# Performance work log

Measured on AMD Instinct MI355X. Metric: run time of the kernel, lower is better.

Reference implementation:

```python
import jax, jax.numpy as jnp
import numpy as np

L, B, T, D, V = 4, 32, 512, 512, 1000


def setup_inputs() -> dict:
    key = jax.random.key(0)
    k0, k1, k2, k3, k4 = jax.random.split(key, 5)
    ids = jax.random.randint(k0, (B, T), 0, V)
    mask = jax.random.randint(k1, (B, T), 0, 2).astype(bool)  # True = valid token
    emb = jax.random.normal(k2, (V, D), dtype=jnp.float32) * 0.1
    W = jax.random.normal(k3, (L, D, 3 * D), dtype=jnp.float32) / np.float32(np.sqrt(D))
    v = jax.random.normal(k4, (L, 2, D), dtype=jnp.float32) * 0.1  # (v_f, v_r) per layer
    b = jnp.zeros((L, 2, D), dtype=jnp.float32)                    # (b_f, b_r) per layer
    return {"ids": ids, "mask": mask, "emb": emb, "W": W, "v": v, "b": b}


def _sru_layer(x, pad, Wl, vf, vr, bf, br):
    # x: [T,B,D] layer input; pad: [T,B,1] bool (True = padded step)
    Tn, Bn, Dn = x.shape
    U = jnp.einsum('tbd,de->tbe', x, Wl).reshape(Tn, Bn, 3, Dn)
    xt, fpre, rpre = U[:, :, 0], U[:, :, 1], U[:, :, 2]

    def step(c, inp):
        xt_t, fp_t, rp_t, x_t, pad_t = inp
        f = jax.nn.sigmoid(fp_t + vf * c + bf)
        r = jax.nn.sigmoid(rp_t + vr * c + br)
        c_new = f * c + (1.0 - f) * xt_t
        h = r * jnp.tanh(c_new) + (1.0 - r) * x_t  # highway (input_size==hidden_size)
        c_out = jnp.where(pad_t, c, c_new)          # padded step: keep state
        h = jnp.where(pad_t, 0.0, h)                # padded step: zero output
        return c_out, h

    c0 = jnp.zeros_like(x[0])  # zero initial hidden state, as in the torch code
    _, h = jax.lax.scan(step, c0, (xt, fpre, rpre, x, pad))
    return h  # [T,B,D]


def reference(ids, mask, emb, W, v, b):
    x = emb[ids]                       # CharEmbedder lookup: [B,T,D]
    x = jnp.transpose(x, (1, 0, 2))    # [T,B,D]  (permute(1,0,2))
    pad = (~mask).T[:, :, None]        # inverted_mask.T -> [T,B,1]
    for l in range(L):
        x = _sru_layer(x, pad, W[l], v[l, 0], v[l, 1], b[l, 0], b[l, 1])
    return jnp.transpose(x, (1, 0, 2))  # back to [B,T,D]
```

## Files before the change

### kernel.cpp

```cpp
#include <hip/hip_runtime.h>
#include <hip/hip_bf16.h>


#define LAYERS 4
#define BB 32
#define TT 512
#define DD 512
#define N3 1536
#define MROWS (TT * BB)
#define WPL ((size_t)DD * N3)
#define SB 32
#define LOG2E 1.4426950408889634f
#define TWOLOG2E 2.8853900817779268f

typedef unsigned short u16;
typedef unsigned int u32;
typedef _Float16 half8 __attribute__((ext_vector_type(8)));
typedef float f32x4 __attribute__((ext_vector_type(4)));

#define SBAR() asm volatile("s_barrier" ::: "memory")
#define WAITVM(n) asm volatile("s_waitcnt vmcnt(" n ")" ::: "memory")

__device__ __forceinline__ float b2f(u16 u) {
  union { unsigned int i; float f; } x;
  x.i = ((unsigned int)u) << 16;
  return x.f;
}
__device__ __forceinline__ u16 f2h(float f) {
  _Float16 h = (_Float16)f;
  return *(u16*)&h;
}
__device__ __forceinline__ float h2f(u16 u) {
  _Float16 h;
  *(u16*)&h = u;
  return (float)h;
}
__device__ __forceinline__ float rcpf(float x) { return __builtin_amdgcn_rcpf(x); }
__device__ __forceinline__ float exp2f_(float x) { return __builtin_amdgcn_exp2f(x); }

__device__ __forceinline__ void async_ld16(const void* g, void* l) {
  __builtin_amdgcn_global_load_lds(
      (const __attribute__((address_space(1))) void*)g,
      (__attribute__((address_space(3))) void*)l, 16, 0, 0);
}
__device__ __forceinline__ void async_ld4(const void* g, void* l) {
  __builtin_amdgcn_global_load_lds(
      (const __attribute__((address_space(1))) void*)g,
      (__attribute__((address_space(3))) void*)l, 4, 0, 0);
}

__global__ void detect_kernel(const u16* __restrict__ emb_u,
                              const int* __restrict__ mask_i,
                              const int* __restrict__ ids_i,
                              int* __restrict__ flags) {
  __shared__ int cnt[3];
  __shared__ int zc;
  int tid = threadIdx.x;
  if (tid < 3) cnt[tid] = 0;
  if (tid == 0) zc = 0;
  __syncthreads();
  int bad = 0, zero_even = 0;
  for (int i = tid; i < 8192; i += 256) {
    u16 u = emb_u[i];
    unsigned e = (u >> 7) & 0xFF;
    if (e >= 0x8F) bad++;
    if ((i & 1) == 0 && u == 0) zero_even++;
  }
  if (bad) atomicAdd(&cnt[0], bad);
  if (zero_even) atomicAdd(&zc, zero_even);
  if (tid < 64) {
    unsigned vv = (unsigned)mask_i[tid];
    if (vv > 1u) atomicAdd(&cnt[1], 1);
  }
  if (tid < 256) {
    if (ids_i[2 * tid + 1] == 0) atomicAdd(&cnt[2], 1);
  }
  __syncthreads();
  if (tid == 0) {
    flags[0] = (cnt[0] > 64 || zc > 3000) ? 1 : 0;
    flags[1] = (cnt[1] > 0) ? 1 : 0;
    flags[2] = (cnt[2] >= 192) ? 1 : 0;
  }
}

__global__ __launch_bounds__(256)
void wprep_kernel(const void* __restrict__ W, u16* __restrict__ W16,
                  const int* __restrict__ flags) {
  __shared__ float tileW[32][33];
  int l = blockIdx.z;
  int k0 = blockIdx.x * 32;
  int n0 = blockIdx.y * 32;
  int tx = threadIdx.x & 31;
  int ty = threadIdx.x >> 5;
  int ff = flags[0];
  const float* Wf = (const float*)W + (size_t)l * WPL;
  const u16* Wb = (const u16*)W + (size_t)l * WPL;
  for (int kk = ty; kk < 32; kk += 8) {
    size_t off = (size_t)(k0 + kk) * N3 + n0 + tx;
    tileW[kk][tx] = ff ? Wf[off] : b2f(Wb[off]);
  }
  __syncthreads();
  u16* outP = W16 + (size_t)l * WPL;
  for (int nn = ty; nn < 32; nn += 8) {
    float x = tileW[tx][nn];
    outP[(size_t)(n0 + nn) * DD + k0 + tx] = f2h(x);
  }
}

__global__ void embed_kernel(const int* __restrict__ ids,
                             const void* __restrict__ emb,
                             u16* __restrict__ X16,
                             const int* __restrict__ flags) {
  int i = blockIdx.x * 256 + threadIdx.x;
  int d = i & (DD - 1);
  int tb = i >> 9;
  int b = tb & (BB - 1);
  int t = tb >> 5;
  int ii = b * TT + t;
  int id = flags[2] ? ids[2 * ii] : ids[ii];
  float val = flags[0] ? ((const float*)emb)[id * DD + d]
                       : b2f(((const u16*)emb)[id * DD + d]);
  X16[i] = f2h(val);
}

__global__ __launch_bounds__(256, 2)
void gemm_kernel(const u16* __restrict__ X16, const u16* __restrict__ W16l,
                 const void* __restrict__ bvec, int layer,
                 const int* __restrict__ flags,
                 u16* __restrict__ U16, int row_base, int chunkM, int nblk) {
  __shared__ u16 ldsA[3][8192];
  __shared__ u16 ldsB[3][4096];
  const int tid = threadIdx.x;
  const int lane = tid & 63, wave = tid >> 6;
  const int wm = wave >> 1, wn = wave & 1;
  const int m16 = lane & 15, quad = lane >> 4;

  const int orig = blockIdx.x;
  const int wg = (orig & 7) * (nblk >> 3) + (orig >> 3);
  const int mt = wg / 12, nt = wg - mt * 12;

  const int arow0 = row_base + mt * 256;
  const int bcol0 = nt * 128;

  const int srow = lane >> 2;
  const int sq = (lane & 3) ^ ((lane >> 3) & 3);
  const u16* pa = X16 + (size_t)(arow0 + wave * 64 + srow) * DD + sq * 8;
  const u16* pb = W16l + (size_t)(bcol0 + wave * 32 + srow) * DD + sq * 8;

  auto stage = [&](int t) {
    const int sl = t % 3;
    const int kv = t * 32;
    u16* da = &ldsA[sl][(wave * 4) * 512];
    const u16* sa = pa + kv;
#pragma unroll
    for (int j = 0; j < 4; ++j)
      async_ld16(sa + (size_t)16 * j * DD, da + j * 512);
    u16* db_ = &ldsB[sl][(wave * 2) * 512];
    const u16* sb = pb + kv;
#pragma unroll
    for (int j = 0; j < 2; ++j)
      async_ld16(sb + (size_t)16 * j * DD, db_ + j * 512);
  };

  f32x4 acc[8][4];
#pragma unroll
  for (int mi = 0; mi < 8; ++mi)
#pragma unroll
    for (int ni = 0; ni < 4; ++ni)
#pragma unroll
      for (int r = 0; r < 4; ++r) acc[mi][ni][r] = 0.f;

  stage(0); stage(1);
  WAITVM("6");
  SBAR();

  const int loff = m16 * 32 + (quad ^ ((m16 >> 1) & 3)) * 8;

#pragma unroll
  for (int t = 0; t < 16; ++t) {
    const int sl = t % 3;
    half8 af[8], bf[4];
#pragma unroll
    for (int i = 0; i < 8; ++i)
      af[i] = *(const half8*)&ldsA[sl][(wm * 8 + i) * 512 + loff];
#pragma unroll
    for (int i = 0; i < 4; ++i)
      bf[i] = *(const half8*)&ldsB[sl][(wn * 4 + i) * 512 + loff];
    if (t + 2 < 16) stage(t + 2);
    __builtin_amdgcn_s_setprio(1);
#pragma unroll
    for (int mi = 0; mi < 8; ++mi)
#pragma unroll
      for (int ni = 0; ni < 4; ++ni)
        acc[mi][ni] = __builtin_amdgcn_mfma_f32_16x16x32_f16(
            af[mi], bf[ni], acc[mi][ni], 0, 0, 0);
    __builtin_amdgcn_s_setprio(0);
    if (t <= 13) WAITVM("6");
    else if (t == 14) WAITVM("0");
    if (t < 15) SBAR();
  }

  const int ff = flags[0];
  const int pl = nt >> 2;
  const int dd0 = (nt & 3) * 128;
  u16* up = U16 + (size_t)pl * chunkM * 512;
  const int r0 = mt * 256 + wm * 128 + quad * 4;
  const int c0 = dd0 + wn * 64 + m16;
  if (pl == 0) {
#pragma unroll
    for (int mi = 0; mi < 8; ++mi)
#pragma unroll
      for (int reg = 0; reg < 4; ++reg) {
        size_t rb = (size_t)(r0 + mi * 16 + reg) * 512 + c0;
#pragma unroll
        for (int ni = 0; ni < 4; ++ni)
          up[rb + ni * 16] = f2h(acc[mi][ni][reg]);
      }
  } else {
    float bias[4];
#pragma unroll
    for (int ni = 0; ni < 4; ++ni) {
      size_t bo = (size_t)layer * 2 * DD + (size_t)(pl - 1) * DD + c0 + ni * 16;
      bias[ni] = ff ? ((const float*)bvec)[bo] : b2f(((const u16*)bvec)[bo]);
    }
#pragma unroll
    for (int mi = 0; mi < 8; ++mi)
#pragma unroll
      for (int reg = 0; reg < 4; ++reg) {
        size_t rb = (size_t)(r0 + mi * 16 + reg) * 512 + c0;
#pragma unroll
        for (int ni = 0; ni < 4; ++ni)
          up[rb + ni * 16] = f2h(-(acc[mi][ni][reg] + bias[ni]) * LOG2E);
      }
  }
}

template <int EMIT>
__global__ __launch_bounds__(448, 1)
void scan_kernel(const u16* __restrict__ U16, float* __restrict__ X,
                 u16* __restrict__ X16,
                 const void* __restrict__ mask_p, const void* __restrict__ vbase,
                 int layer, const int* __restrict__ flags,
                 float* __restrict__ carry, int t0, int nt, int chunkM) {
  __shared__ u16 bufA[2][2][SB][64];
  __shared__ u16 bufB[3][2][SB][64];
  __shared__ float ring[2][2][SB][64];
  __shared__ int msk[TT];
  const int tid = threadIdx.x;
  const int wave = tid >> 6, lane = tid & 63;
  const int idx0 = blockIdx.x * 64;
  const int b = idx0 >> 9;
  const int d0 = idx0 & 511;
  const int ff = flags[0], fm = flags[1];

  const int* mi_ = (const int*)mask_p + b * TT;
  const unsigned char* mb_ = (const unsigned char*)mask_p + b * TT;
  for (int i = tid; i < nt; i += 448) msk[i] = fm ? (int)mb_[t0 + i] : mi_[t0 + i];

  float vfs = 0.f, vrs = 0.f, c = 0.f;
  {
    int d = d0 + lane;
    size_t voff = (size_t)layer * 2 * DD;
    if (wave == 0) {
      float vf = ff ? ((const float*)vbase)[voff + d]
                    : b2f(((const u16*)vbase)[voff + d]);
      vfs = -vf * LOG2E;
      c = (t0 == 0) ? 0.f : carry[idx0 + lane];
    } else if (wave >= 1 && wave <= 4) {
      float vr = ff ? ((const float*)vbase)[voff + DD + d]
                    : b2f(((const u16*)vbase)[voff + DD + d]);
      vrs = -vr * LOG2E;
    }
  }

  const int nbuf = nt / SB;

  auto ld_pair = [&](const u16* rowS, const u16* rowS1, void* ldst) {
    const u32* a0 = (const u32*)rowS;
    const u32* a1 = (const u32*)rowS1;
    const u32* ga = (lane < 32) ? (a0 + lane) : (a1 + (lane - 32));
    async_ld4(ga, ldst);
  };

  auto produceA = [&](int k) {
    int ph = k & 1, tl = k * SB;
    const u16* p0 = U16 + ((size_t)tl * BB + b) * 512 + d0;
    const u16* p1 = p0 + (size_t)chunkM * 512;
#pragma unroll
    for (int s = 0; s < SB; s += 2)
      ld_pair(p0 + (size_t)s * BB * 512, p0 + (size_t)(s + 1) * BB * 512,
              &bufA[ph][0][s][0]);
#pragma unroll
    for (int s = 0; s < SB; s += 2)
      ld_pair(p1 + (size_t)s * BB * 512, p1 + (size_t)(s + 1) * BB * 512,
              &bufA[ph][1][s][0]);
  };
  auto produceB = [&](int k) {
    int ph = k % 3, tl = k * SB;
    const u16* p2 = U16 + 2 * (size_t)chunkM * 512 + ((size_t)tl * BB + b) * 512 + d0;
    const u16* xb = X16 + ((size_t)(t0 + tl) * BB + b) * DD + d0;
#pragma unroll
    for (int s = 0; s < SB; s += 2)
      ld_pair(p2 + (size_t)s * BB * 512, p2 + (size_t)(s + 1) * BB * 512,
              &bufB[ph][0][s][0]);
#pragma unroll
    for (int s = 0; s < SB; s += 2)
      ld_pair(xb + (size_t)s * BB * DD, xb + (size_t)(s + 1) * BB * DD,
              &bufB[ph][1][s][0]);
  };

  float* Xp = X + (size_t)b * TT * DD + d0 + lane;

  auto hphase = [&](int j, int hw) {
    int phc = j & 1, phb = j % 3;
    int sbase = hw * (SB / 4);
#pragma unroll
    for (int si = 0; si < SB / 4; ++si) {
      int s = sbase + si;
      float cprev = ring[phc][0][s][lane];
      float cn = ring[phc][1][s][lane];
      float rps = h2f(bufB[phb][0][s][lane]);
      float xin = h2f(bufB[phb][1][s][lane]);
      int m = msk[j * SB + s];
      float tr = exp2f_(fmaf(vrs, cprev, rps));
      float r = rcpf(1.f + tr);
      float e2 = exp2f_(cn * TWOLOG2E);
      float th = fmaf(-2.f, rcpf(e2 + 1.f), 1.f);
      float h = fmaf(r, th - xin, xin);
      float hout = (m == 0) ? 0.f : h;
      int tg = t0 + j * SB + s;
      if (EMIT)
        X16[((size_t)tg * BB + b) * DD + d0 + lane] = f2h(hout);
      else
        Xp[(size_t)tg * DD] = hout;
    }
  };

  if (wave == 5) produceA(0);
  if (wave == 6) produceB(0);

  for (int k = 0; k < nbuf; ++k) {
    __syncthreads();
    if (wave == 5) {
      if (k + 1 < nbuf) produceA(k + 1);
    } else if (wave == 6) {
      if (k + 1 < nbuf) produceB(k + 1);
    } else if (wave == 0) {
      int ph = k & 1;
#pragma unroll 8
      for (int s = 0; s < SB; ++s) {
        float xt = h2f(bufA[ph][0][s][lane]);
        float fps = h2f(bufA[ph][1][s][lane]);
        float t = exp2f_(fmaf(vfs, c, fps));
        float f = rcpf(1.f + t);
        float cn = fmaf(f, c - xt, xt);
        ring[ph][0][s][lane] = c;
        ring[ph][1][s][lane] = cn;
        c = (msk[k * SB + s] == 0) ? c : cn;
      }
    } else {
      if (k > 0) hphase(k - 1, wave - 1);
    }
  }
  __syncthreads();
  if (wave >= 1 && wave <= 4) hphase(nbuf - 1, wave - 1);
  if (wave == 0) carry[idx0 + lane] = c;
}

__global__ void sentinel_kernel(float* out) { out[threadIdx.x] = 12345.f; }

extern "C" void kernel_launch(void* const* d_in, const int* in_sizes, int n_in,
                              void* d_out, int out_size, void* d_ws, size_t ws_size,
                              hipStream_t stream) {
  const int* ids = (const int*)d_in[0];
  const void* mask = d_in[1];
  const void* emb = d_in[2];
  const void* W = d_in[3];
  const void* v = d_in[4];
  const void* bp = d_in[5];

  char* ws = (char*)d_ws;
  int* flags = (int*)ws;
  float* carry = (float*)(ws + 4096);
  const size_t offX16 = 69632;
  const size_t offW16 = offX16 + (size_t)MROWS * DD * 2;
  const size_t offU = offW16 + (size_t)LAYERS * WPL * 2;
  const size_t perT = (size_t)BB * N3 * 2;

  const int cand[4] = {512, 256, 128, 64};
  int chunkT = 0;
  for (int i = 0; i < 4; ++i) {
    if (ws_size >= offU + (size_t)cand[i] * perT) { chunkT = cand[i]; break; }
  }
  if (!chunkT) {
    sentinel_kernel<<<1, 256, 0, stream>>>((float*)d_out);
    return;
  }
  const int chunkM = chunkT * BB;

  u16* X16 = (u16*)(ws + offX16);
  u16* W16 = (u16*)(ws + offW16);
  u16* U16 = (u16*)(ws + offU);
  float* X = (float*)d_out;

  detect_kernel<<<1, 256, 0, stream>>>((const u16*)emb, (const int*)mask,
                                       (const int*)ids, flags);
  wprep_kernel<<<dim3(16, 48, 4), 256, 0, stream>>>(W, W16, flags);
  embed_kernel<<<MROWS * DD / 256, 256, 0, stream>>>(ids, emb, X16, flags);

  int nch = TT / chunkT;
  for (int l = 0; l < LAYERS; ++l) {
    const u16* W16l = W16 + (size_t)l * WPL;
    for (int ch = 0; ch < nch; ++ch) {
      int t0 = ch * chunkT;
      int nblk = (chunkM / 256) * 12;
      gemm_kernel<<<nblk, 256, 0, stream>>>(X16, W16l, bp, l, flags, U16,
                                            t0 * BB, chunkM, nblk);
      if (l < LAYERS - 1)
        scan_kernel<1><<<BB * DD / 64, 448, 0, stream>>>(U16, X, X16, mask, v, l,
                                                         flags, carry, t0, chunkT,
                                                         chunkM);
      else
        scan_kernel<0><<<BB * DD / 64, 448, 0, stream>>>(U16, X, X16, mask, v, l,
                                                         flags, carry, t0, chunkT,
                                                         chunkM);
    }
  }
}
```

Measured before the change: 348.4 us.

## Fuse GEMM and scan into one launch, pipelining GEMM of next chunk with current scan

GEMM and scan become device functions that share one dynamic LDS buffer. A single fused launch runs the scan of job j-1 and the GEMM of job j in different blocks, with the U buffer double-buffered between the two. The goal is to hide the latency-bound sequential scan behind the projection GEMM and to halve the number of launches. The trade-offs: the largest chunk drops to 256, GEMM blocks run at 448-thread launch bounds with three idle waves that only hit barriers, and the MFMA priority hints are removed.

```diff
diff --git a/kernel.cpp b/kernel.cpp
--- a/kernel.cpp
+++ b/kernel.cpp
@@ -10,6 +10,8 @@
 #define MROWS (TT * BB)
 #define WPL ((size_t)DD * N3)
 #define SB 32
+#define NSCAN 256
+#define SMEM_BYTES 75776
 #define LOG2E 1.4426950408889634f
 #define TWOLOG2E 2.8853900817779268f
 
@@ -123,20 +125,24 @@
   X16[i] = f2h(val);
 }
 
-__global__ __launch_bounds__(256, 2)
-void gemm_kernel(const u16* __restrict__ X16, const u16* __restrict__ W16l,
-                 const void* __restrict__ bvec, int layer,
-                 const int* __restrict__ flags,
-                 u16* __restrict__ U16, int row_base, int chunkM, int nblk) {
-  __shared__ u16 ldsA[3][8192];
-  __shared__ u16 ldsB[3][4096];
+__device__ __forceinline__
+void gemm_body(char* smem, int bid, int nblk,
+               const u16* __restrict__ X16, const u16* __restrict__ W16l,
+               const void* __restrict__ bvec, int layer,
+               const int* __restrict__ flags,
+               u16* __restrict__ U16, int row_base, int chunkM) {
+  u16(*ldsA)[8192] = (u16(*)[8192])smem;
+  u16(*ldsB)[4096] = (u16(*)[4096])(smem + 49152);
   const int tid = threadIdx.x;
   const int lane = tid & 63, wave = tid >> 6;
+  if (wave >= 4) {
+    for (int i = 0; i < 16; ++i) SBAR();
+    return;
+  }
   const int wm = wave >> 1, wn = wave & 1;
   const int m16 = lane & 15, quad = lane >> 4;
 
-  const int orig = blockIdx.x;
-  const int wg = (orig & 7) * (nblk >> 3) + (orig >> 3);
+  const int wg = (bid & 7) * (nblk >> 3) + (bid >> 3);
   const int mt = wg / 12, nt = wg - mt * 12;
 
   const int arow0 = row_base + mt * 256;
@@ -187,14 +193,12 @@
     for (int i = 0; i < 4; ++i)
       bf[i] = *(const half8*)&ldsB[sl][(wn * 4 + i) * 512 + loff];
     if (t + 2 < 16) stage(t + 2);
-    __builtin_amdgcn_s_setprio(1);
 #pragma unroll
     for (int mi = 0; mi < 8; ++mi)
 #pragma unroll
       for (int ni = 0; ni < 4; ++ni)
         acc[mi][ni] = __builtin_amdgcn_mfma_f32_16x16x32_f16(
             af[mi], bf[ni], acc[mi][ni], 0, 0, 0);
-    __builtin_amdgcn_s_setprio(0);
     if (t <= 13) WAITVM("6");
     else if (t == 14) WAITVM("0");
     if (t < 15) SBAR();
@@ -236,19 +240,20 @@
 }
 
 template <int EMIT>
-__global__ __launch_bounds__(448, 1)
-void scan_kernel(const u16* __restrict__ U16, float* __restrict__ X,
-                 u16* __restrict__ X16,
-                 const void* __restrict__ mask_p, const void* __restrict__ vbase,
-                 int layer, const int* __restrict__ flags,
-                 float* __restrict__ carry, int t0, int nt, int chunkM) {
-  __shared__ u16 bufA[2][2][SB][64];
-  __shared__ u16 bufB[3][2][SB][64];
-  __shared__ float ring[2][2][SB][64];
-  __shared__ int msk[TT];
+__device__ __forceinline__
+void scan_body(char* smem, int sbid,
+               const u16* __restrict__ U16, float* __restrict__ X,
+               u16* __restrict__ X16,
+               const void* __restrict__ mask_p, const void* __restrict__ vbase,
+               int layer, const int* __restrict__ flags,
+               float* __restrict__ carry, int t0, int nt, int chunkM) {
+  u16(*bufA)[2][SB][64] = (u16(*)[2][SB][64])smem;
+  u16(*bufB)[2][SB][64] = (u16(*)[2][SB][64])(smem + 16384);
+  float(*ring)[2][SB][64] = (float(*)[2][SB][64])(smem + 40960);
+  int* msk = (int*)(smem + 73728);
   const int tid = threadIdx.x;
   const int wave = tid >> 6, lane = tid & 63;
-  const int idx0 = blockIdx.x * 64;
+  const int idx0 = sbid * 64;
   const int b = idx0 >> 9;
   const int d0 = idx0 & 511;
   const int ff = flags[0], fm = flags[1];
@@ -367,6 +372,25 @@
   if (wave == 0) carry[idx0 + lane] = c;
 }
 
+template <int EMIT>
+__global__ __launch_bounds__(448, 1)
+void fused_kernel(u16* __restrict__ X16, const u16* __restrict__ W16l,
+                  const void* __restrict__ bvec, const void* __restrict__ mask_p,
+                  const void* __restrict__ vbase, const int* __restrict__ flags,
+                  float* __restrict__ X, u16* __restrict__ Ug,
+                  const u16* __restrict__ Us, float* __restrict__ carry,
+                  int glayer, int grow_base, int slayer, int st0,
+                  int nscan, int ngemm, int chunkM, int chunkT) {
+  __shared__ __align__(16) char smem[SMEM_BYTES];
+  if ((int)blockIdx.x < nscan) {
+    scan_body<EMIT>(smem, blockIdx.x, Us, X, X16, mask_p, vbase, slayer,
+                    flags, carry, st0, chunkT, chunkM);
+  } else {
+    gemm_body(smem, blockIdx.x - nscan, ngemm, X16, W16l, bvec, glayer,
+              flags, Ug, grow_base, chunkM);
+  }
+}
+
 __global__ void sentinel_kernel(float* out) { out[threadIdx.x] = 12345.f; }
 
 extern "C" void kernel_launch(void* const* d_in, const int* in_sizes, int n_in,
@@ -384,23 +408,27 @@
   float* carry = (float*)(ws + 4096);
   const size_t offX16 = 69632;
   const size_t offW16 = offX16 + (size_t)MROWS * DD * 2;
-  const size_t offU = offW16 + (size_t)LAYERS * WPL * 2;
+  const size_t offU0 = offW16 + (size_t)LAYERS * WPL * 2;
   const size_t perT = (size_t)BB * N3 * 2;
 
-  const int cand[4] = {512, 256, 128, 64};
   int chunkT = 0;
-  for (int i = 0; i < 4; ++i) {
-    if (ws_size >= offU + (size_t)cand[i] * perT) { chunkT = cand[i]; break; }
+  {
+    const int cand[3] = {256, 128, 64};
+    for (int i = 0; i < 3; ++i) {
+      if (ws_size >= offU0 + 2 * (size_t)cand[i] * perT) { chunkT = cand[i]; break; }
+    }
   }
   if (!chunkT) {
     sentinel_kernel<<<1, 256, 0, stream>>>((float*)d_out);
     return;
   }
   const int chunkM = chunkT * BB;
+  const int nch = TT / chunkT;
 
   u16* X16 = (u16*)(ws + offX16);
   u16* W16 = (u16*)(ws + offW16);
-  u16* U16 = (u16*)(ws + offU);
+  u16* U0 = (u16*)(ws + offU0);
+  u16* U1 = U0 + (size_t)chunkT * (perT / 2);
   float* X = (float*)d_out;
 
   detect_kernel<<<1, 256, 0, stream>>>((const u16*)emb, (const int*)mask,
@@ -408,22 +436,26 @@
   wprep_kernel<<<dim3(16, 48, 4), 256, 0, stream>>>(W, W16, flags);
   embed_kernel<<<MROWS * DD / 256, 256, 0, stream>>>(ids, emb, X16, flags);
 
-  int nch = TT / chunkT;
-  for (int l = 0; l < LAYERS; ++l) {
-    const u16* W16l = W16 + (size_t)l * WPL;
-    for (int ch = 0; ch < nch; ++ch) {
-      int t0 = ch * chunkT;
-      int nblk = (chunkM / 256) * 12;
-      gemm_kernel<<<nblk, 256, 0, stream>>>(X16, W16l, bp, l, flags, U16,
-                                            t0 * BB, chunkM, nblk);
-      if (l < LAYERS - 1)
-        scan_kernel<1><<<BB * DD / 64, 448, 0, stream>>>(U16, X, X16, mask, v, l,
-                                                         flags, carry, t0, chunkT,
-                                                         chunkM);
-      else
-        scan_kernel<0><<<BB * DD / 64, 448, 0, stream>>>(U16, X, X16, mask, v, l,
-                                                         flags, carry, t0, chunkT,
-                                                         chunkM);
-    }
-  }
-}
+  const int njobs = LAYERS * nch;
+  const int nsg = (chunkM / 256) * 12;
+  for (int j = 0; j <= njobs; ++j) {
+    const int ngemm = (j < njobs) ? nsg : 0;
+    const int nscan = (j > 0) ? NSCAN : 0;
+    const int gl = (j < njobs) ? (j / nch) : 0;
+    const int gch = (j < njobs) ? (j % nch) : 0;
+    const int sl = (j > 0) ? ((j - 1) / nch) : 0;
+    const int sch = (j > 0) ? ((j - 1) % nch) : 0;
+    u16* Ug = (j & 1) ? U1 : U0;
+    u16* Us = (j & 1) ? U0 : U1;
+    const u16* W16l = W16 + (size_t)gl * WPL;
+    const int grid = nscan + ngemm;
+    if (j > 0 && sl == LAYERS - 1)
+      fused_kernel<0><<<grid, 448, 0, stream>>>(
+          X16, W16l, bp, mask, v, flags, X, Ug, Us, carry,
+          gl, gch * chunkM, sl, sch * chunkT, nscan, ngemm, chunkM, chunkT);
+    else
+      fused_kernel<1><<<grid, 448, 0, stream>>>(
+          X16, W16l, bp, mask, v, flags, X, Ug, Us, carry,
+          gl, gch * chunkM, sl, sch * chunkT, nscan, ngemm, chunkM, chunkT);
+  }
+}
```

Measured after the change: 396.1 us. 1.14x slower.

## Deepen scan prefetch to two stages with per-wave vmcnt waits

Applied to the files above, without the earlier changes.

Grows the shared staging buffers for the U and X inputs to four phases and has the producer waves issue loads two blocks ahead instead of one. The block-wide __syncthreads is replaced by raw s_barrier, with producer waves waiting only until the older batch of async loads has landed (vmcnt 32). The aim is to hide global-load latency behind the serial recurrence in wave 0. It uses more LDS and relies on exact load-count accounting; a wrong count could introduce races.

```diff
diff --git a/kernel.cpp b/kernel.cpp
--- a/kernel.cpp
+++ b/kernel.cpp
@@ -20,6 +20,7 @@
 
 #define SBAR() asm volatile("s_barrier" ::: "memory")
 #define WAITVM(n) asm volatile("s_waitcnt vmcnt(" n ")" ::: "memory")
+#define WAITLG() asm volatile("s_waitcnt lgkmcnt(0)" ::: "memory")
 
 __device__ __forceinline__ float b2f(u16 u) {
   union { unsigned int i; float f; } x;
@@ -242,8 +243,8 @@
                  const void* __restrict__ mask_p, const void* __restrict__ vbase,
                  int layer, const int* __restrict__ flags,
                  float* __restrict__ carry, int t0, int nt, int chunkM) {
-  __shared__ u16 bufA[2][2][SB][64];
-  __shared__ u16 bufB[3][2][SB][64];
+  __shared__ u16 bufA[4][2][SB][64];
+  __shared__ u16 bufB[4][2][SB][64];
   __shared__ float ring[2][2][SB][64];
   __shared__ int msk[TT];
   const int tid = threadIdx.x;
@@ -283,7 +284,7 @@
   };
 
   auto produceA = [&](int k) {
-    int ph = k & 1, tl = k * SB;
+    int ph = k & 3, tl = k * SB;
     const u16* p0 = U16 + ((size_t)tl * BB + b) * 512 + d0;
     const u16* p1 = p0 + (size_t)chunkM * 512;
 #pragma unroll
@@ -296,7 +297,7 @@
               &bufA[ph][1][s][0]);
   };
   auto produceB = [&](int k) {
-    int ph = k % 3, tl = k * SB;
+    int ph = k & 3, tl = k * SB;
     const u16* p2 = U16 + 2 * (size_t)chunkM * 512 + ((size_t)tl * BB + b) * 512 + d0;
     const u16* xb = X16 + ((size_t)(t0 + tl) * BB + b) * DD + d0;
 #pragma unroll
@@ -312,7 +313,7 @@
   float* Xp = X + (size_t)b * TT * DD + d0 + lane;
 
   auto hphase = [&](int j, int hw) {
-    int phc = j & 1, phb = j % 3;
+    int phc = j & 1, phb = j & 3;
     int sbase = hw * (SB / 4);
 #pragma unroll
     for (int si = 0; si < SB / 4; ++si) {
@@ -336,33 +337,44 @@
     }
   };
 
-  if (wave == 5) produceA(0);
-  if (wave == 6) produceB(0);
+  if (wave == 5) { produceA(0); if (1 < nbuf) produceA(1); }
+  if (wave == 6) { produceB(0); if (1 < nbuf) produceB(1); }
+  WAITLG();
+  if (wave == 5 || wave == 6) {
+    if (1 < nbuf) WAITVM("32");
+    else WAITVM("0");
+  }
+  SBAR();
 
   for (int k = 0; k < nbuf; ++k) {
-    __syncthreads();
     if (wave == 5) {
-      if (k + 1 < nbuf) produceA(k + 1);
+      if (k + 2 < nbuf) { produceA(k + 2); WAITVM("32"); }
+      else WAITVM("0");
+      SBAR();
     } else if (wave == 6) {
-      if (k + 1 < nbuf) produceB(k + 1);
+      if (k + 2 < nbuf) { produceB(k + 2); WAITVM("32"); }
+      else WAITVM("0");
+      SBAR();
     } else if (wave == 0) {
-      int ph = k & 1;
+      int pa_ = k & 3, pr = k & 1;
 #pragma unroll 8
       for (int s = 0; s < SB; ++s) {
-        float xt = h2f(bufA[ph][0][s][lane]);
-        float fps = h2f(bufA[ph][1][s][lane]);
+        float xt = h2f(bufA[pa_][0][s][lane]);
+        float fps = h2f(bufA[pa_][1][s][lane]);
         float t = exp2f_(fmaf(vfs, c, fps));
         float f = rcpf(1.f + t);
         float cn = fmaf(f, c - xt, xt);
-        ring[ph][0][s][lane] = c;
-        ring[ph][1][s][lane] = cn;
+        ring[pr][0][s][lane] = c;
+        ring[pr][1][s][lane] = cn;
         c = (msk[k * SB + s] == 0) ? c : cn;
       }
+      WAITLG();
+      SBAR();
     } else {
       if (k > 0) hphase(k - 1, wave - 1);
+      SBAR();
     }
   }
-  __syncthreads();
   if (wave >= 1 && wave <= 4) hphase(nbuf - 1, wave - 1);
   if (wave == 0) carry[idx0 + lane] = c;
 }
```

Result: slower. 357.4 us (+2.6%).

## Replace warp-specialized LDS pipelined scan with single-wave register-prefetch scan

Applied to the files above, without the earlier changes.

Rewrites the SRU scan kernel so that one 64-thread wave per block does all the work. Each lane computes the f-gate, c update, r-gate and output itself, using a ring of 8 register-prefetched global loads. This drops the producer and consumer waves, the LDS staging buffers and the per-chunk __syncthreads barriers. The cost is one wave per block, so there is less parallelism to hide global load latency, and the serial recurrence now also carries the r-gate and tanh work.

```diff
diff --git a/kernel.cpp b/kernel.cpp
--- a/kernel.cpp
+++ b/kernel.cpp
@@ -9,7 +9,6 @@
 #define N3 1536
 #define MROWS (TT * BB)
 #define WPL ((size_t)DD * N3)
-#define SB 32
 #define LOG2E 1.4426950408889634f
 #define TWOLOG2E 2.8853900817779268f
 
@@ -20,6 +19,7 @@
 
 #define SBAR() asm volatile("s_barrier" ::: "memory")
 #define WAITVM(n) asm volatile("s_waitcnt vmcnt(" n ")" ::: "memory")
+#define WAITLG() asm volatile("s_waitcnt lgkmcnt(0)" ::: "memory")
 
 __device__ __forceinline__ float b2f(u16 u) {
   union { unsigned int i; float f; } x;
@@ -42,11 +42,6 @@
   __builtin_amdgcn_global_load_lds(
       (const __attribute__((address_space(1))) void*)g,
       (__attribute__((address_space(3))) void*)l, 16, 0, 0);
-}
-__device__ __forceinline__ void async_ld4(const void* g, void* l) {
-  __builtin_amdgcn_global_load_lds(
-      (const __attribute__((address_space(1))) void*)g,
-      (__attribute__((address_space(3))) void*)l, 4, 0, 0);
 }
 
 __global__ void detect_kernel(const u16* __restrict__ emb_u,
@@ -236,18 +231,14 @@
 }
 
 template <int EMIT>
-__global__ __launch_bounds__(448, 1)
+__global__ __launch_bounds__(64, 1)
 void scan_kernel(const u16* __restrict__ U16, float* __restrict__ X,
                  u16* __restrict__ X16,
                  const void* __restrict__ mask_p, const void* __restrict__ vbase,
                  int layer, const int* __restrict__ flags,
                  float* __restrict__ carry, int t0, int nt, int chunkM) {
-  __shared__ u16 bufA[2][2][SB][64];
-  __shared__ u16 bufB[3][2][SB][64];
-  __shared__ float ring[2][2][SB][64];
   __shared__ int msk[TT];
-  const int tid = threadIdx.x;
-  const int wave = tid >> 6, lane = tid & 63;
+  const int lane = threadIdx.x;
   const int idx0 = blockIdx.x * 64;
   const int b = idx0 >> 9;
   const int d0 = idx0 & 511;
@@ -255,116 +246,72 @@
 
   const int* mi_ = (const int*)mask_p + b * TT;
   const unsigned char* mb_ = (const unsigned char*)mask_p + b * TT;
-  for (int i = tid; i < nt; i += 448) msk[i] = fm ? (int)mb_[t0 + i] : mi_[t0 + i];
-
-  float vfs = 0.f, vrs = 0.f, c = 0.f;
-  {
-    int d = d0 + lane;
-    size_t voff = (size_t)layer * 2 * DD;
-    if (wave == 0) {
-      float vf = ff ? ((const float*)vbase)[voff + d]
-                    : b2f(((const u16*)vbase)[voff + d]);
-      vfs = -vf * LOG2E;
-      c = (t0 == 0) ? 0.f : carry[idx0 + lane];
-    } else if (wave >= 1 && wave <= 4) {
-      float vr = ff ? ((const float*)vbase)[voff + DD + d]
-                    : b2f(((const u16*)vbase)[voff + DD + d]);
-      vrs = -vr * LOG2E;
-    }
-  }
-
-  const int nbuf = nt / SB;
-
-  auto ld_pair = [&](const u16* rowS, const u16* rowS1, void* ldst) {
-    const u32* a0 = (const u32*)rowS;
-    const u32* a1 = (const u32*)rowS1;
-    const u32* ga = (lane < 32) ? (a0 + lane) : (a1 + (lane - 32));
-    async_ld4(ga, ldst);
-  };
-
-  auto produceA = [&](int k) {
-    int ph = k & 1, tl = k * SB;
-    const u16* p0 = U16 + ((size_t)tl * BB + b) * 512 + d0;
-    const u16* p1 = p0 + (size_t)chunkM * 512;
-#pragma unroll
-    for (int s = 0; s < SB; s += 2)
-      ld_pair(p0 + (size_t)s * BB * 512, p0 + (size_t)(s + 1) * BB * 512,
-              &bufA[ph][0][s][0]);
-#pragma unroll
-    for (int s = 0; s < SB; s += 2)
-      ld_pair(p1 + (size_t)s * BB * 512, p1 + (size_t)(s + 1) * BB * 512,
-              &bufA[ph][1][s][0]);
-  };
-  auto produceB = [&](int k) {
-    int ph = k % 3, tl = k * SB;
-    const u16* p2 = U16 + 2 * (size_t)chunkM * 512 + ((size_t)tl * BB + b) * 512 + d0;
-    const u16* xb = X16 + ((size_t)(t0 + tl) * BB + b) * DD + d0;
-#pragma unroll
-    for (int s = 0; s < SB; s += 2)
-      ld_pair(p2 + (size_t)s * BB * 512, p2 + (size_t)(s + 1) * BB * 512,
-              &bufB[ph][0][s][0]);
-#pragma unroll
-    for (int s = 0; s < SB; s += 2)
-      ld_pair(xb + (size_t)s * BB * DD, xb + (size_t)(s + 1) * BB * DD,
-              &bufB[ph][1][s][0]);
-  };
-
-  float* Xp = X + (size_t)b * TT * DD + d0 + lane;
-
-  auto hphase = [&](int j, int hw) {
-    int phc = j & 1, phb = j % 3;
-    int sbase = hw * (SB / 4);
-#pragma unroll
-    for (int si = 0; si < SB / 4; ++si) {
-      int s = sbase + si;
-      float cprev = ring[phc][0][s][lane];
-      float cn = ring[phc][1][s][lane];
-      float rps = h2f(bufB[phb][0][s][lane]);
-      float xin = h2f(bufB[phb][1][s][lane]);
-      int m = msk[j * SB + s];
-      float tr = exp2f_(fmaf(vrs, cprev, rps));
-      float r = rcpf(1.f + tr);
-      float e2 = exp2f_(cn * TWOLOG2E);
-      float th = fmaf(-2.f, rcpf(e2 + 1.f), 1.f);
-      float h = fmaf(r, th - xin, xin);
-      float hout = (m == 0) ? 0.f : h;
-      int tg = t0 + j * SB + s;
-      if (EMIT)
-        X16[((size_t)tg * BB + b) * DD + d0 + lane] = f2h(hout);
-      else
-        Xp[(size_t)tg * DD] = hout;
+  for (int i = lane; i < nt; i += 64) msk[i] = fm ? (int)mb_[t0 + i] : mi_[t0 + i];
+  WAITLG();
+
+  const int d = d0 + lane;
+  const size_t voff = (size_t)layer * 2 * DD;
+  const float vf = ff ? ((const float*)vbase)[voff + d]
+                      : b2f(((const u16*)vbase)[voff + d]);
+  const float vr = ff ? ((const float*)vbase)[voff + DD + d]
+                      : b2f(((const u16*)vbase)[voff + DD + d]);
+  const float vfs = -vf * LOG2E;
+  const float vrs = -vr * LOG2E;
+  float c = (t0 == 0) ? 0.f : carry[idx0 + lane];
+
+  const size_t SU = (size_t)BB * 512;
+  const u16* p0 = U16 + (size_t)b * 512 + d0 + lane;
+  const u16* p1 = p0 + (size_t)chunkM * 512;
+  const u16* p2 = p1 + (size_t)chunkM * 512;
+  const u16* px = X16 + ((size_t)t0 * BB + b) * DD + d0 + lane;
+  u16* pxw = X16 + ((size_t)t0 * BB + b) * DD + d0 + lane;
+  float* pX = X + ((size_t)b * TT + t0) * DD + d0 + lane;
+
+  constexpr int PF = 8;
+  u16 bx[PF], bp[PF], bq[PF], bi[PF];
+#pragma unroll
+  for (int j = 0; j < PF; ++j) {
+    bx[j] = p0[(size_t)j * SU];
+    bp[j] = p1[(size_t)j * SU];
+    bq[j] = p2[(size_t)j * SU];
+    bi[j] = px[(size_t)j * SU];
+  }
+
+  auto stepblk = [&](int tb, bool pre) {
+#pragma unroll
+    for (int j = 0; j < PF; ++j) {
+      const int t = tb + j;
+      const float xt = h2f(bx[j]);
+      const float fps = h2f(bp[j]);
+      const float rps = h2f(bq[j]);
+      const float xi = h2f(bi[j]);
+      if (pre) {
+        bx[j] = p0[(size_t)(t + PF) * SU];
+        bp[j] = p1[(size_t)(t + PF) * SU];
+        bq[j] = p2[(size_t)(t + PF) * SU];
+        bi[j] = px[(size_t)(t + PF) * SU];
+      }
+      const int m = msk[t];
+      const float tf = exp2f_(fmaf(vfs, c, fps));
+      const float f = rcpf(1.f + tf);
+      const float cn = fmaf(f, c - xt, xt);
+      const float tr = exp2f_(fmaf(vrs, c, rps));
+      const float r = rcpf(1.f + tr);
+      const float e2 = exp2f_(cn * TWOLOG2E);
+      const float th = fmaf(-2.f, rcpf(e2 + 1.f), 1.f);
+      const float h = fmaf(r, th - xi, xi);
+      const float hout = (m == 0) ? 0.f : h;
+      if (EMIT) pxw[(size_t)t * SU] = f2h(hout);
+      else pX[(size_t)t * DD] = hout;
+      c = (m == 0) ? c : cn;
     }
   };
 
-  if (wave == 5) produceA(0);
-  if (wave == 6) produceB(0);
-
-  for (int k = 0; k < nbuf; ++k) {
-    __syncthreads();
-    if (wave == 5) {
-      if (k + 1 < nbuf) produceA(k + 1);
-    } else if (wave == 6) {
-      if (k + 1 < nbuf) produceB(k + 1);
-    } else if (wave == 0) {
-      int ph = k & 1;
-#pragma unroll 8
-      for (int s = 0; s < SB; ++s) {
-        float xt = h2f(bufA[ph][0][s][lane]);
-        float fps = h2f(bufA[ph][1][s][lane]);
-        float t = exp2f_(fmaf(vfs, c, fps));
-        float f = rcpf(1.f + t);
-        float cn = fmaf(f, c - xt, xt);
-        ring[ph][0][s][lane] = c;
-        ring[ph][1][s][lane] = cn;
-        c = (msk[k * SB + s] == 0) ? c : cn;
-      }
-    } else {
-      if (k > 0) hphase(k - 1, wave - 1);
-    }
-  }
-  __syncthreads();
-  if (wave >= 1 && wave <= 4) hphase(nbuf - 1, wave - 1);
-  if (wave == 0) carry[idx0 + lane] = c;
+  int tb = 0;
+  for (; tb < nt - PF; tb += PF) stepblk(tb, true);
+  stepblk(tb, false);
+
+  carry[idx0 + lane] = c;
 }
 
 __global__ void sentinel_kernel(float* out) { out[threadIdx.x] = 12345.f; }
@@ -417,13 +364,13 @@
       gemm_kernel<<<nblk, 256, 0, stream>>>(X16, W16l, bp, l, flags, U16,
                                             t0 * BB, chunkM, nblk);
       if (l < LAYERS - 1)
-        scan_kernel<1><<<BB * DD / 64, 448, 0, stream>>>(U16, X, X16, mask, v, l,
-                                                         flags, carry, t0, chunkT,
-                                                         chunkM);
+        scan_kernel<1><<<BB * DD / 64, 64, 0, stream>>>(U16, X, X16, mask, v, l,
+                                                        flags, carry, t0, chunkT,
+                                                        chunkM);
       else
-        scan_kernel<0><<<BB * DD / 64, 448, 0, stream>>>(U16, X, X16, mask, v, l,
-                                                         flags, carry, t0, chunkT,
-                                                         chunkM);
+        scan_kernel<0><<<BB * DD / 64, 64, 0, stream>>>(U16, X, X16, mask, v, l,
+                                                        flags, carry, t0, chunkT,
+                                                        chunkM);
     }
   }
 }
```

New measurement: 483.3 us. 1.39x slower.
